# Optimization experiments

Measured on AMD Instinct MI355X. Metric: run time of the kernel, lower is better.

Reference implementation:

```python
import jax, jax.numpy as jnp
import numpy as np

B, N, IN_F = 2, 512, 10
SET_FEATS = [128, 128, 64]
HIDDEN = 256
D2 = 2 * SET_FEATS[-1]


def _init_linear(key, fout, fin):
    kw, kb = jax.random.split(key)
    bound = 1.0 / np.sqrt(fin)
    W = jax.random.uniform(kw, (fout, fin), jnp.float32, -bound, bound)
    b = jax.random.uniform(kb, (fout,), jnp.float32, -bound, bound)
    return W, b


def setup_inputs() -> dict:
    key = jax.random.key(0)
    keys = jax.random.split(key, 6)
    x = jax.random.normal(keys[0], (B, N, IN_F), jnp.float32)
    Ws0, bs0 = _init_linear(keys[1], SET_FEATS[0], IN_F)
    Ws1, bs1 = _init_linear(keys[2], SET_FEATS[1], SET_FEATS[0])
    Ws2, bs2 = _init_linear(keys[3], SET_FEATS[2], SET_FEATS[1])
    Wp0, bp0 = _init_linear(keys[4], HIDDEN, D2)
    Wp1, bp1 = _init_linear(keys[5], 1, HIDDEN)
    return {"x": x, "Ws0": Ws0, "bs0": bs0, "Ws1": Ws1, "bs1": bs1,
            "Ws2": Ws2, "bs2": bs2, "Wp0": Wp0, "bp0": bp0,
            "Wp1": Wp1, "bp1": bp1}


def reference(x, Ws0, bs0, Ws1, bs1, Ws2, bs2, Wp0, bp0, Wp1, bp1):
    # x: [B, N, in_features] -> transpose(2,1) -> [B, C, N]
    u = jnp.transpose(x, (0, 2, 1))
    # set_model: per-point MLP (1x1 conv stack), ReLU after each layer
    for W, b in ((Ws0, bs0), (Ws1, bs1), (Ws2, bs2)):
        u = jax.nn.relu(jnp.einsum('fc,bcn->bfn', W, u) + b[None, :, None])
    # pairwise block: cat([u_j broadcast, u_i broadcast], dim=1) -> [B, 2d, N, N]
    # fused into the first suffix 1x1 conv: out[b,f,i,j] = Wa@u[:,j] + Wb@u[:,i] + b
    d = Wp0.shape[1] // 2
    Wa, Wb = Wp0[:, :d], Wp0[:, d:]
    ha = jnp.einsum('fc,bcn->bfn', Wa, u)  # depends on j (m1[b,c,i,j] = u[b,c,j])
    hb = jnp.einsum('fc,bcn->bfn', Wb, u)  # depends on i (m2[b,c,i,j] = u[b,c,i])
    h = jax.nn.relu(ha[:, :, None, :] + hb[:, :, :, None] + bp0[None, :, None, None])
    # final 1x1 conv to 1 channel, no activation
    out = jnp.einsum('fc,bcij->bfij', Wp1, h) + bp1[None, :, None, None]
    return out  # [B, 1, N, N]
```

## Files before the change

kernel.cpp:

```cpp
#include <hip/hip_runtime.h>

#define BB 2
#define NN 512
#define INF 10
#define FPAD 260

static __device__ __forceinline__ float dot4(float4 w, float4 v, float acc) {
    acc = fmaf(w.x, v.x, acc);
    acc = fmaf(w.y, v.y, acc);
    acc = fmaf(w.z, v.z, acc);
    acc = fmaf(w.w, v.w, acc);
    return acc;
}

__global__ __launch_bounds__(256) void k_points(
    const float* __restrict__ x,
    const float* __restrict__ Ws0, const float* __restrict__ bs0,
    const float* __restrict__ Ws1, const float* __restrict__ bs1,
    const float* __restrict__ Ws2, const float* __restrict__ bs2,
    const float* __restrict__ Wp0, const float* __restrict__ bp0,
    float* __restrict__ haT, float* __restrict__ hbT)
{
    __shared__ __align__(16) float xs[4][INF];
    __shared__ __align__(16) float u0s[4][128];
    __shared__ __align__(16) float u1s[4][128];
    __shared__ __align__(16) float u2s[4][64];

    const int t  = threadIdx.x;
    const int p0 = blockIdx.x * 4;

    if (t < 4 * INF) {
        int p = t / INF, c = t % INF;
        xs[p][c] = x[(p0 + p) * INF + c];
    }
    __syncthreads();

    {
        const int f = t & 127, ph = t >> 7;
        float a0 = bs0[f], a1 = a0;
        #pragma unroll
        for (int c = 0; c < INF; ++c) {
            float w = Ws0[f * INF + c];
            a0 = fmaf(w, xs[ph * 2 + 0][c], a0);
            a1 = fmaf(w, xs[ph * 2 + 1][c], a1);
        }
        u0s[ph * 2 + 0][f] = fmaxf(a0, 0.f);
        u0s[ph * 2 + 1][f] = fmaxf(a1, 0.f);
    }
    __syncthreads();

    {
        const int f = t & 127, ph = t >> 7;
        float a0 = bs1[f], a1 = a0;
        const float4* wv = (const float4*)(Ws1 + f * 128);
        #pragma unroll 8
        for (int c4 = 0; c4 < 32; ++c4) {
            float4 w  = wv[c4];
            float4 x0 = *(const float4*)&u0s[ph * 2 + 0][c4 * 4];
            float4 x1 = *(const float4*)&u0s[ph * 2 + 1][c4 * 4];
            a0 = dot4(w, x0, a0);
            a1 = dot4(w, x1, a1);
        }
        u1s[ph * 2 + 0][f] = fmaxf(a0, 0.f);
        u1s[ph * 2 + 1][f] = fmaxf(a1, 0.f);
    }
    __syncthreads();

    {
        const int f = t & 63, p = t >> 6;
        float a = bs2[f];
        const float4* wv = (const float4*)(Ws2 + f * 128);
        #pragma unroll 8
        for (int c4 = 0; c4 < 32; ++c4) {
            float4 w  = wv[c4];
            float4 xv = *(const float4*)&u1s[p][c4 * 4];
            a = dot4(w, xv, a);
        }
        u2s[p][f] = fmaxf(a, 0.f);
    }
    __syncthreads();

    {
        const int f = t;
        float ah[4], bh[4];
        const float bb = bp0[f];
        #pragma unroll
        for (int p = 0; p < 4; ++p) { ah[p] = 0.f; bh[p] = bb; }
        const float4* wv = (const float4*)(Wp0 + f * 128);
        #pragma unroll 4
        for (int c4 = 0; c4 < 16; ++c4) {
            float4 wa = wv[c4];
            float4 wb = wv[16 + c4];
            #pragma unroll
            for (int p = 0; p < 4; ++p) {
                float4 u = *(const float4*)&u2s[p][c4 * 4];
                ah[p] = dot4(wa, u, ah[p]);
                bh[p] = dot4(wb, u, bh[p]);
            }
        }
        #pragma unroll
        for (int p = 0; p < 4; ++p) {
            haT[(size_t)(p0 + p) * 256 + f] = ah[p];
            hbT[(size_t)(p0 + p) * 256 + f] = bh[p];
        }
    }
}

__global__ __launch_bounds__(256) void k_outer(
    const float* __restrict__ haT, const float* __restrict__ hbT,
    const float* __restrict__ Wp1, const float* __restrict__ bp1,
    float* __restrict__ out)
{
    __shared__ __align__(16) float sA[32][FPAD];
    __shared__ __align__(16) float sB[32][FPAD];
    __shared__ __align__(16) float sW[256];

    const int t  = threadIdx.x;
    const int jb = blockIdx.x * 32;
    const int ib = blockIdx.y * 32;
    const int b  = blockIdx.z;

    const float4* gA = (const float4*)(haT + ((size_t)b * NN + jb) * 256);
    const float4* gB = (const float4*)(hbT + ((size_t)b * NN + ib) * 256);
    #pragma unroll
    for (int k = 0; k < 8; ++k) {
        int idx = t + 256 * k;
        int row = idx >> 6, f4 = idx & 63;
        float4 va = gA[row * 64 + f4];
        float4 vb = gB[row * 64 + f4];
        *(float4*)&sA[row][f4 * 4] = va;
        *(float4*)&sB[row][f4 * 4] = vb;
    }
    if (t < 64) *(float4*)&sW[t * 4] = ((const float4*)Wp1)[t];
    __syncthreads();

    const int lane = t & 63, wid = t >> 6;
    const int li = lane >> 3, lj = lane & 7;
    const int wr = wid >> 1, wc = wid & 1;
    const int i0 = wr * 16 + li * 2;
    const int j0 = wc * 16 + lj * 2;

    const float* A0 = &sA[j0][0];
    const float* A1 = &sA[j0 + 1][0];
    const float* B0 = &sB[i0][0];
    const float* B1 = &sB[i0 + 1][0];

    float acc00 = 0.f, acc01 = 0.f, acc10 = 0.f, acc11 = 0.f;

#define STEP(comp)                                                     \
    {                                                                  \
        float wk = w.comp;                                             \
        acc00 = fmaf(wk, fmaxf(a0.comp + b0.comp, 0.f), acc00);        \
        acc01 = fmaf(wk, fmaxf(a1.comp + b0.comp, 0.f), acc01);        \
        acc10 = fmaf(wk, fmaxf(a0.comp + b1.comp, 0.f), acc10);        \
        acc11 = fmaf(wk, fmaxf(a1.comp + b1.comp, 0.f), acc11);        \
    }

    #pragma unroll 4
    for (int f = 0; f < 256; f += 4) {
        float4 a0 = *(const float4*)(A0 + f);
        float4 a1 = *(const float4*)(A1 + f);
        float4 b0 = *(const float4*)(B0 + f);
        float4 b1 = *(const float4*)(B1 + f);
        float4 w  = *(const float4*)(sW + f);
        STEP(x) STEP(y) STEP(z) STEP(w)
    }
#undef STEP

    const float bv = bp1[0];
    const int gi = ib + i0, gj = jb + j0;
    float* o = out + (size_t)b * NN * NN;
    float2 r0 = { acc00 + bv, acc01 + bv };
    float2 r1 = { acc10 + bv, acc11 + bv };
    *(float2*)&o[(size_t)gi * NN + gj]       = r0;
    *(float2*)&o[(size_t)(gi + 1) * NN + gj] = r1;
}

extern "C" void kernel_launch(void* const* d_in, const int* in_sizes, int n_in,
                              void* d_out, int out_size, void* d_ws, size_t ws_size,
                              hipStream_t stream) {
    const float* x   = (const float*)d_in[0];
    const float* Ws0 = (const float*)d_in[1];
    const float* bs0 = (const float*)d_in[2];
    const float* Ws1 = (const float*)d_in[3];
    const float* bs1 = (const float*)d_in[4];
    const float* Ws2 = (const float*)d_in[5];
    const float* bs2 = (const float*)d_in[6];
    const float* Wp0 = (const float*)d_in[7];
    const float* bp0 = (const float*)d_in[8];
    const float* Wp1 = (const float*)d_in[9];
    const float* bp1 = (const float*)d_in[10];

    float* haT = (float*)d_ws;
    float* hbT = haT + (size_t)BB * NN * 256;

    k_points<<<dim3(BB * NN / 4), dim3(256), 0, stream>>>(
        x, Ws0, bs0, Ws1, bs1, Ws2, bs2, Wp0, bp0, haT, hbT);

    k_outer<<<dim3(NN / 32, NN / 32, BB), dim3(256), 0, stream>>>(
        haT, hbT, Wp1, bp1, (float*)d_out);
}
```

Before: 102.7 us.

## Split hidden dim across blocks with 4x4 register tiles and atomic accumulation

```diff
diff --git a/kernel.cpp b/kernel.cpp
--- a/kernel.cpp
+++ b/kernel.cpp
@@ -3,7 +3,6 @@
 #define BB 2
 #define NN 512
 #define INF 10
-#define FPAD 260
 
 static __device__ __forceinline__ float dot4(float4 w, float4 v, float acc) {
     acc = fmaf(w.x, v.x, acc);
@@ -19,7 +18,8 @@
     const float* __restrict__ Ws1, const float* __restrict__ bs1,
     const float* __restrict__ Ws2, const float* __restrict__ bs2,
     const float* __restrict__ Wp0, const float* __restrict__ bp0,
-    float* __restrict__ haT, float* __restrict__ hbT)
+    float* __restrict__ haT, float* __restrict__ hbT,
+    float* __restrict__ out, const float* __restrict__ bp1)
 {
     __shared__ __align__(16) float xs[4][INF];
     __shared__ __align__(16) float u0s[4][128];
@@ -28,6 +28,15 @@
 
     const int t  = threadIdx.x;
     const int p0 = blockIdx.x * 4;
+
+    {
+        const float bv = bp1[0];
+        const float4 b4 = { bv, bv, bv, bv };
+        float4* o4 = (float4*)out;
+        const int gt = blockIdx.x * 256 + t;
+        o4[gt * 2 + 0] = b4;
+        o4[gt * 2 + 1] = b4;
+    }
 
     if (t < 4 * INF) {
         int p = t / INF, c = t % INF;
@@ -108,72 +117,77 @@
 
 __global__ __launch_bounds__(256) void k_outer(
     const float* __restrict__ haT, const float* __restrict__ hbT,
-    const float* __restrict__ Wp1, const float* __restrict__ bp1,
-    float* __restrict__ out)
+    const float* __restrict__ Wp1, float* __restrict__ out)
 {
-    __shared__ __align__(16) float sA[32][FPAD];
-    __shared__ __align__(16) float sB[32][FPAD];
-    __shared__ __align__(16) float sW[256];
+    __shared__ __align__(16) float sA[64 * 64];
+    __shared__ __align__(16) float sB[64 * 64];
+    __shared__ __align__(16) float sW[64];
 
     const int t  = threadIdx.x;
-    const int jb = blockIdx.x * 32;
-    const int ib = blockIdx.y * 32;
-    const int b  = blockIdx.z;
-
-    const float4* gA = (const float4*)(haT + ((size_t)b * NN + jb) * 256);
-    const float4* gB = (const float4*)(hbT + ((size_t)b * NN + ib) * 256);
+    const int jb = blockIdx.x * 64;
+    const int ib = blockIdx.y * 64;
+    const int b  = blockIdx.z >> 2;
+    const int f0 = (blockIdx.z & 3) * 64;
+
     #pragma unroll
-    for (int k = 0; k < 8; ++k) {
-        int idx = t + 256 * k;
-        int row = idx >> 6, f4 = idx & 63;
-        float4 va = gA[row * 64 + f4];
-        float4 vb = gB[row * 64 + f4];
-        *(float4*)&sA[row][f4 * 4] = va;
-        *(float4*)&sB[row][f4 * 4] = vb;
-    }
-    if (t < 64) *(float4*)&sW[t * 4] = ((const float4*)Wp1)[t];
+    for (int k = 0; k < 4; ++k) {
+        const int u  = t + 256 * k;
+        const int r  = u >> 4;
+        const int f4 = u & 15;
+        const int fs = f4 ^ ((r >> 2) & 7);
+        float4 va = ((const float4*)(haT + ((size_t)(b * NN + jb + r)) * 256 + f0))[f4];
+        float4 vb = ((const float4*)(hbT + ((size_t)(b * NN + ib + r)) * 256 + f0))[f4];
+        *(float4*)&sA[r * 64 + fs * 4] = va;
+        *(float4*)&sB[r * 64 + fs * 4] = vb;
+    }
+    if (t < 16) *(float4*)&sW[t * 4] = ((const float4*)(Wp1 + f0))[t];
     __syncthreads();
 
     const int lane = t & 63, wid = t >> 6;
     const int li = lane >> 3, lj = lane & 7;
     const int wr = wid >> 1, wc = wid & 1;
-    const int i0 = wr * 16 + li * 2;
-    const int j0 = wc * 16 + lj * 2;
-
-    const float* A0 = &sA[j0][0];
-    const float* A1 = &sA[j0 + 1][0];
-    const float* B0 = &sB[i0][0];
-    const float* B1 = &sB[i0 + 1][0];
-
-    float acc00 = 0.f, acc01 = 0.f, acc10 = 0.f, acc11 = 0.f;
-
-#define STEP(comp)                                                     \
-    {                                                                  \
-        float wk = w.comp;                                             \
-        acc00 = fmaf(wk, fmaxf(a0.comp + b0.comp, 0.f), acc00);        \
-        acc01 = fmaf(wk, fmaxf(a1.comp + b0.comp, 0.f), acc01);        \
-        acc10 = fmaf(wk, fmaxf(a0.comp + b1.comp, 0.f), acc10);        \
-        acc11 = fmaf(wk, fmaxf(a1.comp + b1.comp, 0.f), acc11);        \
-    }
-
-    #pragma unroll 4
-    for (int f = 0; f < 256; f += 4) {
-        float4 a0 = *(const float4*)(A0 + f);
-        float4 a1 = *(const float4*)(A1 + f);
-        float4 b0 = *(const float4*)(B0 + f);
-        float4 b1 = *(const float4*)(B1 + f);
-        float4 w  = *(const float4*)(sW + f);
-        STEP(x) STEP(y) STEP(z) STEP(w)
-    }
-#undef STEP
-
-    const float bv = bp1[0];
+    const int i0 = wr * 32 + li * 4;
+    const int j0 = wc * 32 + lj * 4;
+
+    const int swa = lj << 4;
+    const int swb = li << 4;
+    const char* baseA = (const char*)&sA[j0 * 64];
+    const char* baseB = (const char*)&sB[i0 * 64];
+
+    float acc[4][4] = {{0.f}};
+
+    #pragma unroll
+    for (int g = 0; g < 16; ++g) {
+        const float4 w = *(const float4*)&sW[g * 4];
+        const int xa = (g << 4) ^ swa;
+        const int xb = (g << 4) ^ swb;
+        float4 av[4], bv[4];
+        #pragma unroll
+        for (int k = 0; k < 4; ++k) {
+            av[k] = *(const float4*)(baseA + k * 256 + xa);
+            bv[k] = *(const float4*)(baseB + k * 256 + xb);
+        }
+        #pragma unroll
+        for (int di = 0; di < 4; ++di) {
+            #pragma unroll
+            for (int dj = 0; dj < 4; ++dj) {
+                acc[di][dj] = fmaf(w.x, fmaxf(av[dj].x + bv[di].x, 0.f), acc[di][dj]);
+                acc[di][dj] = fmaf(w.y, fmaxf(av[dj].y + bv[di].y, 0.f), acc[di][dj]);
+                acc[di][dj] = fmaf(w.z, fmaxf(av[dj].z + bv[di].z, 0.f), acc[di][dj]);
+                acc[di][dj] = fmaf(w.w, fmaxf(av[dj].w + bv[di].w, 0.f), acc[di][dj]);
+            }
+        }
+    }
+
+    float* o = out + (size_t)b * NN * NN;
     const int gi = ib + i0, gj = jb + j0;
-    float* o = out + (size_t)b * NN * NN;
-    float2 r0 = { acc00 + bv, acc01 + bv };
-    float2 r1 = { acc10 + bv, acc11 + bv };
-    *(float2*)&o[(size_t)gi * NN + gj]       = r0;
-    *(float2*)&o[(size_t)(gi + 1) * NN + gj] = r1;
+    #pragma unroll
+    for (int di = 0; di < 4; ++di) {
+        #pragma unroll
+        for (int dj = 0; dj < 4; ++dj) {
+            atomicAdd(&o[(size_t)(gi + di) * NN + (gj + dj)], acc[di][dj]);
+        }
+    }
 }
 
 extern "C" void kernel_launch(void* const* d_in, const int* in_sizes, int n_in,
@@ -195,8 +209,8 @@
     float* hbT = haT + (size_t)BB * NN * 256;
 
     k_points<<<dim3(BB * NN / 4), dim3(256), 0, stream>>>(
-        x, Ws0, bs0, Ws1, bs1, Ws2, bs2, Wp0, bp0, haT, hbT);
-
-    k_outer<<<dim3(NN / 32, NN / 32, BB), dim3(256), 0, stream>>>(
-        haT, hbT, Wp1, bp1, (float*)d_out);
-}
+        x, Ws0, bs0, Ws1, bs1, Ws2, bs2, Wp0, bp0, haT, hbT, (float*)d_out, bp1);
+
+    k_outer<<<dim3(NN / 64, NN / 64, BB * 4), dim3(256), 0, stream>>>(
+        haT, hbT, Wp1, (float*)d_out);
+}
```

Measured after the change: 131.8 us. +28.3%, slower.

## Retile outer kernel to 64x32 with XOR-swizzled shared memory and feature chunking

Applied to the files above, without the earlier changes.

```diff
diff --git a/kernel.cpp b/kernel.cpp
--- a/kernel.cpp
+++ b/kernel.cpp
@@ -3,7 +3,9 @@
 #define BB 2
 #define NN 512
 #define INF 10
-#define FPAD 260
+#define TI 64
+#define TJ 32
+#define FCH 128
 
 static __device__ __forceinline__ float dot4(float4 w, float4 v, float acc) {
     acc = fmaf(w.x, v.x, acc);
@@ -111,69 +113,88 @@
     const float* __restrict__ Wp1, const float* __restrict__ bp1,
     float* __restrict__ out)
 {
-    __shared__ __align__(16) float sA[32][FPAD];
-    __shared__ __align__(16) float sB[32][FPAD];
-    __shared__ __align__(16) float sW[256];
+    __shared__ __align__(512) float sA[TJ * FCH];
+    __shared__ __align__(512) float sB[TI * FCH];
 
     const int t  = threadIdx.x;
-    const int jb = blockIdx.x * 32;
-    const int ib = blockIdx.y * 32;
+    const int jb = blockIdx.x * TJ;
+    const int ib = blockIdx.y * TI;
     const int b  = blockIdx.z;
 
-    const float4* gA = (const float4*)(haT + ((size_t)b * NN + jb) * 256);
-    const float4* gB = (const float4*)(hbT + ((size_t)b * NN + ib) * 256);
+    const int lane = t & 63, w = t >> 6;
+    const int lj = lane & 15;
+    const int li = lane >> 4;
+    const int j0 = lj * 2;
+    const int i0 = w * 16 + li * 4;
+    const int xa = lj;
+    const int xb = w * 4 + li;
+
+    const uintptr_t aB0 = (uintptr_t)sA + (size_t)j0 * (FCH * 4) + (xa << 4);
+    const uintptr_t aB1 = aB0 + FCH * 4;
+    uintptr_t bBs[4];
     #pragma unroll
-    for (int k = 0; k < 8; ++k) {
-        int idx = t + 256 * k;
-        int row = idx >> 6, f4 = idx & 63;
-        float4 va = gA[row * 64 + f4];
-        float4 vb = gB[row * 64 + f4];
-        *(float4*)&sA[row][f4 * 4] = va;
-        *(float4*)&sB[row][f4 * 4] = vb;
-    }
-    if (t < 64) *(float4*)&sW[t * 4] = ((const float4*)Wp1)[t];
-    __syncthreads();
-
-    const int lane = t & 63, wid = t >> 6;
-    const int li = lane >> 3, lj = lane & 7;
-    const int wr = wid >> 1, wc = wid & 1;
-    const int i0 = wr * 16 + li * 2;
-    const int j0 = wc * 16 + lj * 2;
-
-    const float* A0 = &sA[j0][0];
-    const float* A1 = &sA[j0 + 1][0];
-    const float* B0 = &sB[i0][0];
-    const float* B1 = &sB[i0 + 1][0];
-
-    float acc00 = 0.f, acc01 = 0.f, acc10 = 0.f, acc11 = 0.f;
-
-#define STEP(comp)                                                     \
-    {                                                                  \
-        float wk = w.comp;                                             \
-        acc00 = fmaf(wk, fmaxf(a0.comp + b0.comp, 0.f), acc00);        \
-        acc01 = fmaf(wk, fmaxf(a1.comp + b0.comp, 0.f), acc01);        \
-        acc10 = fmaf(wk, fmaxf(a0.comp + b1.comp, 0.f), acc10);        \
-        acc11 = fmaf(wk, fmaxf(a1.comp + b1.comp, 0.f), acc11);        \
-    }
-
-    #pragma unroll 4
-    for (int f = 0; f < 256; f += 4) {
-        float4 a0 = *(const float4*)(A0 + f);
-        float4 a1 = *(const float4*)(A1 + f);
-        float4 b0 = *(const float4*)(B0 + f);
-        float4 b1 = *(const float4*)(B1 + f);
-        float4 w  = *(const float4*)(sW + f);
-        STEP(x) STEP(y) STEP(z) STEP(w)
-    }
-#undef STEP
-
-    const float bv = bp1[0];
-    const int gi = ib + i0, gj = jb + j0;
+    for (int di = 0; di < 4; ++di)
+        bBs[di] = (uintptr_t)sB + (size_t)(i0 + di) * (FCH * 4) + (xb << 4);
+
+    float acc[4][2];
+    #pragma unroll
+    for (int di = 0; di < 4; ++di) { acc[di][0] = 0.f; acc[di][1] = 0.f; }
+
+    const int sp = t & 31;
+
+    for (int ph = 0; ph < 2; ++ph) {
+        const int f0 = ph * FCH;
+        if (ph) __syncthreads();
+
+        #pragma unroll
+        for (int k = 0; k < 4; ++k) {
+            const int r  = (t >> 5) + 8 * k;
+            const int sg = sp ^ ((r >> 1) & 15);
+            float4 v = *(const float4*)(haT + ((size_t)(b * NN + jb + r)) * 256 + f0 + sg * 4);
+            *(float4*)&sA[r * FCH + sp * 4] = v;
+        }
+        #pragma unroll
+        for (int k = 0; k < 8; ++k) {
+            const int r  = (t >> 5) + 8 * k;
+            const int sg = sp ^ ((r >> 2) & 15);
+            float4 v = *(const float4*)(hbT + ((size_t)(b * NN + ib + r)) * 256 + f0 + sg * 4);
+            *(float4*)&sB[r * FCH + sp * 4] = v;
+        }
+        __syncthreads();
+
+        const float4* wg = (const float4*)(Wp1 + f0);
+
+        #pragma unroll 8
+        for (int g = 0; g < 32; ++g) {
+            const float4 w4 = wg[g];
+            const uintptr_t gx = (uintptr_t)(g << 4);
+            const float4 a0 = *(const float4*)(aB0 ^ gx);
+            const float4 a1 = *(const float4*)(aB1 ^ gx);
+            float4 bv[4];
+            #pragma unroll
+            for (int di = 0; di < 4; ++di) bv[di] = *(const float4*)(bBs[di] ^ gx);
+
+            #pragma unroll
+            for (int di = 0; di < 4; ++di) {
+                acc[di][0] = fmaf(w4.x, fmaxf(a0.x + bv[di].x, 0.f), acc[di][0]);
+                acc[di][1] = fmaf(w4.x, fmaxf(a1.x + bv[di].x, 0.f), acc[di][1]);
+                acc[di][0] = fmaf(w4.y, fmaxf(a0.y + bv[di].y, 0.f), acc[di][0]);
+                acc[di][1] = fmaf(w4.y, fmaxf(a1.y + bv[di].y, 0.f), acc[di][1]);
+                acc[di][0] = fmaf(w4.z, fmaxf(a0.z + bv[di].z, 0.f), acc[di][0]);
+                acc[di][1] = fmaf(w4.z, fmaxf(a1.z + bv[di].z, 0.f), acc[di][1]);
+                acc[di][0] = fmaf(w4.w, fmaxf(a0.w + bv[di].w, 0.f), acc[di][0]);
+                acc[di][1] = fmaf(w4.w, fmaxf(a1.w + bv[di].w, 0.f), acc[di][1]);
+            }
+        }
+    }
+
+    const float bias = bp1[0];
     float* o = out + (size_t)b * NN * NN;
-    float2 r0 = { acc00 + bv, acc01 + bv };
-    float2 r1 = { acc10 + bv, acc11 + bv };
-    *(float2*)&o[(size_t)gi * NN + gj]       = r0;
-    *(float2*)&o[(size_t)(gi + 1) * NN + gj] = r1;
+    #pragma unroll
+    for (int di = 0; di < 4; ++di) {
+        float2 v = { acc[di][0] + bias, acc[di][1] + bias };
+        *(float2*)&o[(size_t)(ib + i0 + di) * NN + (jb + j0)] = v;
+    }
 }
 
 extern "C" void kernel_launch(void* const* d_in, const int* in_sizes, int n_in,
@@ -197,6 +218,6 @@
     k_points<<<dim3(BB * NN / 4), dim3(256), 0, stream>>>(
         x, Ws0, bs0, Ws1, bs1, Ws2, bs2, Wp0, bp0, haT, hbT);
 
-    k_outer<<<dim3(NN / 32, NN / 32, BB), dim3(256), 0, stream>>>(
+    k_outer<<<dim3(NN / TJ, NN / TI, BB), dim3(256), 0, stream>>>(
         haT, hbT, Wp1, bp1, (float*)d_out);
 }
```

After: 108.7 us. 1.06x slower.
